# Kernel tuning notes

Hardware: AMD Instinct MI355X
Metric: run time of the kernel (lower is better)

Reference implementation:

```python
import jax, jax.numpy as jnp
import numpy as np


def setup_inputs() -> dict:
    key = jax.random.key(0)
    k1, k2, k3 = jax.random.split(key, 3)
    bs, r, d = 4, 4096, 64
    G = jax.random.uniform(k1, (bs, d), dtype=jnp.float32)          # eigenvalues (non-negative)
    V = jax.random.normal(k2, (bs, r, d), dtype=jnp.float32)        # eigenvectors / spectral embedding
    weights = jax.random.uniform(k3, (1,), dtype=jnp.float32)       # learned scalar t
    return {"G": G, "V": V, "weights": weights}


def reference(G, V, weights):
    # Original: eVs = diag(max(G,0)^(2t)); y = E@eVs@Phi2^T + Phi2@eVs@E^T - 2*Phi@eVs@Phi^T
    # Since eVs is diagonal, this is the weighted pairwise squared distance:
    # y[b,i,j] = sum_k w[b,k] * (V[b,i,k] - V[b,j,k])^2 with w = max(G,0)^(2t).
    t = weights[0]
    w = jnp.maximum(G, jnp.zeros_like(G)) ** (2.0 * t)   # (bs, d)
    Vw = V * w[:, None, :]                               # (bs, r, d) elementwise diag scaling
    s = jnp.sum(Vw * V, axis=-1)                         # (bs, r): weighted squared norms
    cross = jnp.einsum('brd,bsd->brs', Vw, V)            # (bs, r, r)
    y = s[:, :, None] + s[:, None, :] - 2.0 * cross
    return y
```

## Files before the change

kernel.cpp:

```cpp
#include <hip/hip_runtime.h>
#include <hip/hip_bf16.h>


typedef __attribute__((ext_vector_type(8))) short bf16x8;
typedef __attribute__((ext_vector_type(4))) float f32x4;

constexpr int BS = 4, R = 4096, D = 64;
constexpr int LS = 260;

__device__ __forceinline__ void barrier_lds_only() {
    asm volatile("s_waitcnt lgkmcnt(0)" ::: "memory");
    __builtin_amdgcn_sched_barrier(0);
    __builtin_amdgcn_s_barrier();
    __builtin_amdgcn_sched_barrier(0);
}

__global__ __launch_bounds__(256) void prep_kernel(
    const float* __restrict__ G, const float* __restrict__ V,
    const float* __restrict__ wt,
    __hip_bfloat16* __restrict__ u_bf, float* __restrict__ s)
{
    int row  = blockIdx.x * 4 + (threadIdx.x >> 6);
    int lane = threadIdx.x & 63;
    if (row >= BS * R) return;
    int b = row / R;

    float t  = wt[0];
    float g  = fmaxf(G[b * D + lane], 0.0f);
    float sw = powf(g, t);
    float u  = sw * V[(size_t)row * D + lane];

    __hip_bfloat16 ub = __float2bfloat16(u);
    u_bf[(size_t)row * D + lane] = ub;

    float uf   = __bfloat162float(ub);
    float prod = uf * uf;
    #pragma unroll
    for (int off = 32; off; off >>= 1) prod += __shfl_down(prod, off);
    if (lane == 0) s[row] = prod;
}

__global__ __launch_bounds__(512, 3) void dist_kernel(
    const short* __restrict__ U, const float* __restrict__ s,
    float* __restrict__ out)
{
    __shared__ float lds[32 * LS];

    int lane = threadIdx.x & 63;
    int wave = threadIdx.x >> 6;
    int wr   = wave >> 2;
    int wc   = wave & 3;

    int b  = blockIdx.z;
    int jb = blockIdx.x * 256;
    int i0 = blockIdx.y * 128;

    const short* Ap = U + ((size_t)b * R + i0 + wr * 64) * D;
    const short* Bp = U + ((size_t)b * R + jb + wc * 64) * D;
    const float* sb = s + (size_t)b * R;

    int lrow = lane & 15;
    int kgrp = lane >> 4;

    bf16x8 a[4][2];
    #pragma unroll
    for (int rb = 0; rb < 4; ++rb)
        #pragma unroll
        for (int ks = 0; ks < 2; ++ks)
            a[rb][ks] = *(const bf16x8*)(Ap + (rb * 16 + lrow) * D + ks * 32 + kgrp * 8);

    f32x4 acc[4][4];
    #pragma unroll
    for (int rb = 0; rb < 4; ++rb)
        #pragma unroll
        for (int jt = 0; jt < 4; ++jt)
            acc[rb][jt] = f32x4{0.f, 0.f, 0.f, 0.f};

    #pragma unroll
    for (int jt = 0; jt < 4; ++jt) {
        const short* Bt = Bp + jt * 16 * D;
        bf16x8 b0 = *(const bf16x8*)(Bt + lrow * D +      kgrp * 8);
        bf16x8 b1 = *(const bf16x8*)(Bt + lrow * D + 32 + kgrp * 8);
        #pragma unroll
        for (int rb = 0; rb < 4; ++rb) {
            acc[rb][jt] = __builtin_amdgcn_mfma_f32_16x16x32_bf16(a[rb][0], b0, acc[rb][jt], 0, 0, 0);
            acc[rb][jt] = __builtin_amdgcn_mfma_f32_16x16x32_bf16(a[rb][1], b1, acc[rb][jt], 0, 0, 0);
        }
    }

    float si_lane = sb[i0 + wr * 64 + lane];

    float* outb = out + ((size_t)b * R + i0) * R + jb;

    #pragma unroll
    for (int c = 0; c < 4; ++c) {
        if (wr == (c >> 1)) {
            #pragma unroll
            for (int rb2 = 0; rb2 < 2; ++rb2) {
                int rb = (c & 1) * 2 + rb2;
                #pragma unroll
                for (int rg = 0; rg < 4; ++rg) {
                    int rl = rb * 16 + kgrp * 4 + rg;
                    int rc = rl - (c & 1) * 32;
                    float si = __shfl(si_lane, rl);
                    #pragma unroll
                    for (int jt = 0; jt < 4; ++jt) {
                        float sj = sb[jb + wc * 64 + jt * 16 + lrow];
                        float y  = si + sj - 2.0f * acc[rb][jt][rg];
                        lds[rc * LS + wc * 64 + jt * 16 + lrow] = y;
                    }
                }
            }
        }
        barrier_lds_only();

        #pragma unroll
        for (int r = 0; r < 4; ++r) {
            int rl = wave * 4 + r;
            f32x4 v = *(const f32x4*)&lds[rl * LS + lane * 4];
            __builtin_nontemporal_store(v,
                (f32x4*)(outb + (size_t)(c * 32 + rl) * R + lane * 4));
        }
        if (c < 3) barrier_lds_only();
    }
}

extern "C" void kernel_launch(void* const* d_in, const int* in_sizes, int n_in,
                              void* d_out, int out_size, void* d_ws, size_t ws_size,
                              hipStream_t stream) {
    const float* G  = (const float*)d_in[0];
    const float* V  = (const float*)d_in[1];
    const float* wt = (const float*)d_in[2];
    float* out = (float*)d_out;

    char* ws = (char*)d_ws;
    __hip_bfloat16* u_bf = (__hip_bfloat16*)ws;
    float*          s    = (float*)        (ws + (size_t)BS * R * D * 2);

    prep_kernel<<<BS * R / 4, 256, 0, stream>>>(G, V, wt, u_bf, s);

    dim3 grid(R / 256, R / 128, BS);
    dist_kernel<<<grid, 512, 0, stream>>>((const short*)u_bf, s, out);
}
```

Measured before the change: 66.02 us.

## Make dist kernel persistent per 32-row strip, looping over column chunks

Each block now owns a 32-row strip of one batch and loops over all 4096 columns in 512-wide chunks. A fragments and s_i stay in registers across the whole strip, and all 8 waves split the columns instead of sharing a 2x4 row/column grid. The grid shrinks from 2048 to 512 blocks and the LDS staging buffer doubles to 32x516 floats. The occupancy hint of 3 blocks per CU is dropped. The aim is to amortise block launch and A loads and to make longer contiguous row stores, at the cost of fewer blocks for load balancing and a serialized compute-then-store loop inside each block.

```diff
diff --git a/kernel.cpp b/kernel.cpp
--- a/kernel.cpp
+++ b/kernel.cpp
@@ -6,7 +6,8 @@
 typedef __attribute__((ext_vector_type(4))) float f32x4;
 
 constexpr int BS = 4, R = 4096, D = 64;
-constexpr int LS = 260;
+constexpr int JS = 512;
+constexpr int LS = JS + 4;
 
 __device__ __forceinline__ void barrier_lds_only() {
     asm volatile("s_waitcnt lgkmcnt(0)" ::: "memory");
@@ -40,7 +41,7 @@
     if (lane == 0) s[row] = prod;
 }
 
-__global__ __launch_bounds__(512, 3) void dist_kernel(
+__global__ __launch_bounds__(512) void dist_kernel(
     const short* __restrict__ U, const float* __restrict__ s,
     float* __restrict__ out)
 {
@@ -48,67 +49,61 @@
 
     int lane = threadIdx.x & 63;
     int wave = threadIdx.x >> 6;
-    int wr   = wave >> 2;
-    int wc   = wave & 3;
-
-    int b  = blockIdx.z;
-    int jb = blockIdx.x * 256;
-    int i0 = blockIdx.y * 128;
-
-    const short* Ap = U + ((size_t)b * R + i0 + wr * 64) * D;
-    const short* Bp = U + ((size_t)b * R + jb + wc * 64) * D;
-    const float* sb = s + (size_t)b * R;
-
     int lrow = lane & 15;
     int kgrp = lane >> 4;
 
-    bf16x8 a[4][2];
+    int bid = blockIdx.x;
+    int b   = bid >> 7;
+    int i0  = (bid & 127) * 32;
+
+    const short* Ap = U + ((size_t)b * R + i0) * D;
+    const short* Bb = U + (size_t)b * R * D;
+    const float* sb = s + (size_t)b * R;
+
+    bf16x8 a[2][2];
     #pragma unroll
-    for (int rb = 0; rb < 4; ++rb)
+    for (int rb = 0; rb < 2; ++rb)
         #pragma unroll
         for (int ks = 0; ks < 2; ++ks)
             a[rb][ks] = *(const bf16x8*)(Ap + (rb * 16 + lrow) * D + ks * 32 + kgrp * 8);
 
-    f32x4 acc[4][4];
-    #pragma unroll
-    for (int rb = 0; rb < 4; ++rb)
+    float si_lane = sb[i0 + (lane & 31)];
+    float* outb = out + ((size_t)b * R + i0) * R;
+
+    for (int jx = 0; jx < R / JS; ++jx) {
+        int jw = jx * JS + wave * 64;
+
+        f32x4 acc[2][4];
         #pragma unroll
-        for (int jt = 0; jt < 4; ++jt)
-            acc[rb][jt] = f32x4{0.f, 0.f, 0.f, 0.f};
+        for (int rb = 0; rb < 2; ++rb)
+            #pragma unroll
+            for (int jt = 0; jt < 4; ++jt)
+                acc[rb][jt] = f32x4{0.f, 0.f, 0.f, 0.f};
 
-    #pragma unroll
-    for (int jt = 0; jt < 4; ++jt) {
-        const short* Bt = Bp + jt * 16 * D;
-        bf16x8 b0 = *(const bf16x8*)(Bt + lrow * D +      kgrp * 8);
-        bf16x8 b1 = *(const bf16x8*)(Bt + lrow * D + 32 + kgrp * 8);
+        const short* Bp = Bb + (size_t)jw * D;
         #pragma unroll
-        for (int rb = 0; rb < 4; ++rb) {
-            acc[rb][jt] = __builtin_amdgcn_mfma_f32_16x16x32_bf16(a[rb][0], b0, acc[rb][jt], 0, 0, 0);
-            acc[rb][jt] = __builtin_amdgcn_mfma_f32_16x16x32_bf16(a[rb][1], b1, acc[rb][jt], 0, 0, 0);
+        for (int jt = 0; jt < 4; ++jt) {
+            const short* Bt = Bp + jt * 16 * D;
+            bf16x8 b0 = *(const bf16x8*)(Bt + lrow * D +      kgrp * 8);
+            bf16x8 b1 = *(const bf16x8*)(Bt + lrow * D + 32 + kgrp * 8);
+            #pragma unroll
+            for (int rb = 0; rb < 2; ++rb) {
+                acc[rb][jt] = __builtin_amdgcn_mfma_f32_16x16x32_bf16(a[rb][0], b0, acc[rb][jt], 0, 0, 0);
+                acc[rb][jt] = __builtin_amdgcn_mfma_f32_16x16x32_bf16(a[rb][1], b1, acc[rb][jt], 0, 0, 0);
+            }
         }
-    }
 
-    float si_lane = sb[i0 + wr * 64 + lane];
-
-    float* outb = out + ((size_t)b * R + i0) * R + jb;
-
-    #pragma unroll
-    for (int c = 0; c < 4; ++c) {
-        if (wr == (c >> 1)) {
+        #pragma unroll
+        for (int rb = 0; rb < 2; ++rb) {
             #pragma unroll
-            for (int rb2 = 0; rb2 < 2; ++rb2) {
-                int rb = (c & 1) * 2 + rb2;
+            for (int rg = 0; rg < 4; ++rg) {
+                int rl = rb * 16 + kgrp * 4 + rg;
+                float si = __shfl(si_lane, rl);
                 #pragma unroll
-                for (int rg = 0; rg < 4; ++rg) {
-                    int rl = rb * 16 + kgrp * 4 + rg;
-                    int rc = rl - (c & 1) * 32;
-                    float si = __shfl(si_lane, rl);
-                    #pragma unroll
-                    for (int jt = 0; jt < 4; ++jt) {
-                        float sj = sb[jb + wc * 64 + jt * 16 + lrow];
-                        float y  = si + sj - 2.0f * acc[rb][jt][rg];
-                        lds[rc * LS + wc * 64 + jt * 16 + lrow] = y;
-                    }
+                for (int jt = 0; jt < 4; ++jt) {
+                    float sj = sb[jw + jt * 16 + lrow];
+                    float y  = si + sj - 2.0f * acc[rb][jt][rg];
+                    lds[rl * LS + wave * 64 + jt * 16 + lrow] = y;
                 }
             }
         }
@@ -117,11 +112,14 @@
         #pragma unroll
         for (int r = 0; r < 4; ++r) {
             int rl = wave * 4 + r;
-            f32x4 v = *(const f32x4*)&lds[rl * LS + lane * 4];
-            __builtin_nontemporal_store(v,
-                (f32x4*)(outb + (size_t)(c * 32 + rl) * R + lane * 4));
+            #pragma unroll
+            for (int t = 0; t < 2; ++t) {
+                f32x4 v = *(const f32x4*)&lds[rl * LS + t * 256 + lane * 4];
+                __builtin_nontemporal_store(v,
+                    (f32x4*)(outb + (size_t)rl * R + jx * JS + t * 256 + lane * 4));
+            }
         }
-        if (c < 3) barrier_lds_only();
+        barrier_lds_only();
     }
 }
 
@@ -139,6 +137,5 @@
 
     prep_kernel<<<BS * R / 4, 256, 0, stream>>>(G, V, wt, u_bf, s);
 
-    dim3 grid(R / 256, R / 128, BS);
-    dist_kernel<<<grid, 512, 0, stream>>>((const short*)u_bf, s, out);
+    dist_kernel<<<BS * (R / 32), 512, 0, stream>>>((const short*)u_bf, s, out);
 }
```

New measurement: 77.31 us. +17.1%, slower.
